# Performance work log

Measured on AMD Instinct MI355X. Metric: run time of the kernel, lower is better.

Reference implementation:

```python
import jax, jax.numpy as jnp
import numpy as np

EPS = 1e-5
NHEAD = 8

def layernorm(x, g, b):
    m = x.mean(-1, keepdims=True)
    v = ((x - m) ** 2).mean(-1, keepdims=True)
    return (x - m) * jax.lax.rsqrt(v + EPS) * g + b


def setup_inputs() -> dict:
    key = jax.random.key(0)
    ks = jax.random.split(key, 20)
    D, F, K, G, NC, FF, B = 768, 2048, 100, 10, 1000, 2048, 128
    s = lambda k, shape, scale: jax.random.normal(k, shape, jnp.float32) * scale
    return {
        "x": s(ks[0], (B, F, 7, 7), 1.0),
        "W_embed": s(ks[1], (F, D), 0.02), "b_embed": jnp.zeros((D,), jnp.float32),
        "query_embed": s(ks[2], (K, D), 1.0),
        "wq": s(ks[3], (D, D), 0.03), "wk": s(ks[4], (D, D), 0.03), "wv": s(ks[5], (D, D), 0.03),
        "bq": jnp.zeros((D,), jnp.float32), "bk": jnp.zeros((D,), jnp.float32), "bv": jnp.zeros((D,), jnp.float32),
        "wo": s(ks[6], (D, D), 0.03), "bo": jnp.zeros((D,), jnp.float32),
        "w1": s(ks[7], (D, FF), 0.03), "b1": jnp.zeros((FF,), jnp.float32),
        "w2": s(ks[8], (FF, D), 0.02), "b2": jnp.zeros((D,), jnp.float32),
        "g1": jnp.ones((D,), jnp.float32), "be1": jnp.zeros((D,), jnp.float32),
        "g2": jnp.ones((D,), jnp.float32), "be2": jnp.zeros((D,), jnp.float32),
        "g3": jnp.ones((D,), jnp.float32), "be3": jnp.zeros((D,), jnp.float32),
        "dup_pool": s(ks[9], (K, D, G), 0.03),
        "dup_bias": jnp.zeros((NC,), jnp.float32),
    }


def reference(x, W_embed, b_embed, query_embed, wq, wk, wv, bq, bk, bv, wo, bo,
              w1, b1, w2, b2, g1, be1, g2, be2, g3, be3, dup_pool, dup_bias):
    B = x.shape[0]
    D = W_embed.shape[1]
    H = NHEAD
    hd = D // H
    num_classes = dup_bias.shape[0]

    # [B, 2048, 7, 7] -> [B, 49, 2048] -> [B, 49, 768], relu
    mem = x.reshape(B, x.shape[1], -1).transpose(0, 2, 1)
    mem = jax.nn.relu(mem @ W_embed + b_embed)          # (B, S, D)

    # queries broadcast to batch (batch-first internally)
    tgt = jnp.broadcast_to(query_embed[None], (B,) + query_embed.shape)  # (B, K, D)

    # tgt = tgt + dropout1(tgt) -> 2*tgt in eval; then norm1
    tgt = layernorm(2.0 * tgt, g1, be1)

    # cross multi-head attention: Q=tgt, K=V=mem
    q = (tgt @ wq + bq).reshape(B, -1, H, hd)
    k = (mem @ wk + bk).reshape(B, -1, H, hd)
    v = (mem @ wv + bv).reshape(B, -1, H, hd)
    scores = jnp.einsum("bkhd,bshd->bhks", q, k) / jnp.sqrt(jnp.float32(hd))
    attn = jax.nn.softmax(scores, axis=-1)
    ctx = jnp.einsum("bhks,bshd->bkhd", attn, v).reshape(B, -1, D)
    attn_out = ctx @ wo + bo

    tgt = layernorm(tgt + attn_out, g2, be2)

    # FFN
    ff = jax.nn.relu(tgt @ w1 + b1) @ w2 + b2
    h = layernorm(tgt + ff, g3, be3)                    # (B, K, D)

    # GroupFC: per-group matmul, batched as one einsum
    out_extrap = jnp.einsum("bkd,kdg->bkg", h, dup_pool)  # (B, K, G)
    logits = out_extrap.reshape(B, -1)[:, :num_classes] + dup_bias
    return logits
```

## Files before the change

### kernel.cpp

```cpp
#include <hip/hip_runtime.h>
#include <math.h>

#define D_MODEL 768
#define HEADS   8
#define HDIM    96
#define SEQ     49
#define KQ      100
#define NB      128
#define FDIM    2048
#define FFD     2048
#define GRP     10
#define NCLS    1000

typedef unsigned short ushort_t;
typedef unsigned int uint_t;
typedef __attribute__((ext_vector_type(8))) short short8;
typedef __attribute__((ext_vector_type(4))) float f32x4;

__device__ __forceinline__ float bf2f(ushort_t u) {
    uint_t x = ((uint_t)u) << 16;
    return __uint_as_float(x);
}
__device__ __forceinline__ ushort_t f2bf(float f) {
    uint_t x = __float_as_uint(f);
    x += 0x7fffu + ((x >> 16) & 1u);
    return (ushort_t)(x >> 16);
}

__device__ __forceinline__ void gld_lds16(const void* g, void* l) {
    __builtin_amdgcn_global_load_lds(
        (const __attribute__((address_space(1))) unsigned int*)g,
        (__attribute__((address_space(3))) unsigned int*)l, 16, 0, 0);
}

template <int MT>
__device__ __forceinline__ void gemm_body(
    const ushort_t* __restrict__ A, const ushort_t* __restrict__ Bt,
    const float* __restrict__ bias, const float* __restrict__ bias2,
    ushort_t* __restrict__ C, ushort_t* __restrict__ C2,
    int M, int N, int K, int nsplit, int relu, float scale,
    const ushort_t* __restrict__ resid, int rmode, int r, int c)
{
    constexpr int BM  = MT * 32;
    constexpr int ACH = MT * 4;
    constexpr int NCH = (ACH + 16) / 4;
    constexpr int CTS = 132;

    __shared__ ushort_t smem[BM * 64 + 128 * 64];
    ushort_t* As = smem;
    ushort_t* Bs = smem + BM * 64;

    const int tid  = threadIdx.x;
    const int w    = tid >> 6;
    const int lane = tid & 63;
    const int quad = lane >> 4;
    const int l16  = lane & 15;

    const int rowBase = r * BM;
    const int nBase   = c * 128;
    const int wr = (w >> 1) * (MT * 16);
    const int wc = (w & 1) * 64;

    const float* biasb;
    ushort_t* Cb;
    int coff, ldcb;
    if (nBase < nsplit) { biasb = bias;  Cb = C;  coff = 0;      ldcb = nsplit; }
    else                { biasb = bias2; Cb = C2; coff = nsplit; ldcb = N - nsplit; }

    f32x4 acc[MT][4];
#pragma unroll
    for (int i = 0; i < MT; i++)
#pragma unroll
        for (int j = 0; j < 4; j++) acc[i][j] = (f32x4){0.f, 0.f, 0.f, 0.f};

    const int lrow = lane >> 3;
    const int ksub = ((lane & 7) ^ ((lane >> 3) & 7)) * 8;

    const ushort_t* gp[NCH];
    ushort_t* lp[NCH];
#pragma unroll
    for (int i = 0; i < NCH; i++) {
        int ch = w + 4 * i;
        if (ch < ACH) {
            int rr = min(rowBase + ch * 8 + lrow, M - 1);
            gp[i] = A + (size_t)rr * K + ksub;
            lp[i] = As + ch * 512 + lane * 8;
        } else {
            int cb = ch - ACH;
            int rr = nBase + cb * 8 + lrow;
            gp[i] = Bt + (size_t)rr * K + ksub;
            lp[i] = Bs + cb * 512 + lane * 8;
        }
    }

    const int swl = l16 & 7;

    for (int k0 = 0; k0 < K; k0 += 64) {
#pragma unroll
        for (int i = 0; i < NCH; i++) gld_lds16(gp[i] + k0, lp[i]);
        __syncthreads();

#pragma unroll
        for (int s = 0; s < 2; s++) {
            const int ks = ((4 * s + quad) ^ swl) * 8;
            short8 af[MT], bfr[4];
#pragma unroll
            for (int mt = 0; mt < MT; mt++)
                af[mt] = *(const short8*)(As + (wr + mt * 16 + l16) * 64 + ks);
#pragma unroll
            for (int nt = 0; nt < 4; nt++)
                bfr[nt] = *(const short8*)(Bs + (wc + nt * 16 + l16) * 64 + ks);
#pragma unroll
            for (int mt = 0; mt < MT; mt++)
#pragma unroll
                for (int nt = 0; nt < 4; nt++)
                    acc[mt][nt] = __builtin_amdgcn_mfma_f32_16x16x32_bf16(
                        af[mt], bfr[nt], acc[mt][nt], 0, 0, 0);
        }
        __syncthreads();
    }

    ushort_t* Ct = smem;
#pragma unroll
    for (int nt = 0; nt < 4; nt++) {
        const int colg = nBase + wc + nt * 16 + l16;
        const int col  = colg - coff;
        const float bv = biasb[col];
#pragma unroll
        for (int mt = 0; mt < MT; mt++) {
#pragma unroll
            for (int rg = 0; rg < 4; rg++) {
                const int lr  = wr + mt * 16 + quad * 4 + rg;
                const int row = rowBase + lr;
                float v = (acc[mt][nt][rg] + bv) * scale;
                if (relu) v = fmaxf(v, 0.f);
                if (rmode && row < M) {
                    int rrow = (rmode == 2) ? (row % KQ) : row;
                    v += bf2f(resid[(size_t)rrow * D_MODEL + col]);
                }
                Ct[lr * CTS + wc + nt * 16 + l16] = f2bf(v);
            }
        }
    }
    __syncthreads();

    const int ocol = (tid & 15) * 8;
    const int ceff = nBase - coff + ocol;
#pragma unroll
    for (int i = 0; i < BM / 16; i++) {
        const int lr  = i * 16 + (tid >> 4);
        const int row = rowBase + lr;
        if (row < M) {
            short8 vv = *(const short8*)(Ct + lr * CTS + ocol);
            *(short8*)(Cb + (size_t)row * ldcb + ceff) = vv;
        }
    }
}

__device__ __forceinline__ void xcd_remap(int bx, int by, int nx, int NY,
                                          int& r, int& c)
{
    const int bid = by * nx + bx;
    const int NYmain = NY & ~7;
    const int Tmain = NYmain * nx;
    if (bid < Tmain) {
        const int grp = bid / (8 * nx);
        const int rem = bid - grp * 8 * nx;
        r = grp * 8 + (rem & 7);
        c = rem >> 3;
    } else {
        const int rem = bid - Tmain;
        r = NYmain + rem / nx;
        c = rem - (rem / nx) * nx;
    }
}

template <int MT>
__global__ __launch_bounds__(256, 4) void gemm_bf16(
    const ushort_t* __restrict__ A, const ushort_t* __restrict__ Bt,
    const float* __restrict__ bias, const float* __restrict__ bias2,
    ushort_t* __restrict__ C, ushort_t* __restrict__ C2,
    int M, int N, int K, int nsplit, int relu, float scale,
    const ushort_t* __restrict__ resid, int rmode)
{
    int r, c;
    xcd_remap(blockIdx.x, blockIdx.y, gridDim.x, gridDim.y, r, c);
    gemm_body<MT>(A, Bt, bias, bias2, C, C2, M, N, K, nsplit, relu, scale,
                  resid, rmode, r, c);
}

__global__ __launch_bounds__(256, 4) void gemm_kv_qb(
    const ushort_t* __restrict__ mem, const ushort_t* __restrict__ wkt,
    const float* __restrict__ bk, const float* __restrict__ bv,
    ushort_t* __restrict__ kb, ushort_t* __restrict__ vb,
    const ushort_t* __restrict__ tgt, const ushort_t* __restrict__ wqt,
    const float* __restrict__ bq, ushort_t* __restrict__ qb,
    float qscale)
{
    const int bx = blockIdx.x, by = blockIdx.y;
    const ushort_t *A, *Bt;
    const float *bias, *bias2;
    ushort_t *C, *C2;
    int M, N, K, ns, r, c;
    float scale;
    if (by < 98) {
        xcd_remap(bx, by, 12, 98, r, c);
        A = mem; Bt = wkt; bias = bk; bias2 = bv; C = kb; C2 = vb;
        M = 6272; N = 1536; K = 768; ns = 768; scale = 1.f;
    } else {
        if (bx >= 6) return;
        r = by - 98; c = bx;
        A = tgt; Bt = wqt; bias = bq; bias2 = bq; C = qb; C2 = qb;
        M = KQ; N = 768; K = 768; ns = 768; scale = qscale;
    }
    gemm_body<2>(A, Bt, bias, bias2, C, C2, M, N, K, ns, 0, scale,
                 nullptr, 0, r, c);
}

__global__ __launch_bounds__(256) void prep_all(
    const float* __restrict__ We, const float* __restrict__ wq,
    const float* __restrict__ wk, const float* __restrict__ wv,
    const float* __restrict__ wo, const float* __restrict__ w1,
    const float* __restrict__ w2, const float* __restrict__ x,
    ushort_t* __restrict__ Wet, ushort_t* __restrict__ wqt,
    ushort_t* __restrict__ wkt, ushort_t* __restrict__ wvt,
    ushort_t* __restrict__ wot, ushort_t* __restrict__ w1t,
    ushort_t* __restrict__ w2t, ushort_t* __restrict__ xb,
    const float* __restrict__ qe, const float* __restrict__ g1,
    const float* __restrict__ be1, ushort_t* __restrict__ tgt)
{
    __shared__ __align__(16) char smem[25600];
    int t = blockIdx.x;
    if (t < 1728) {
        float* tile = (float*)smem;
        const float* src; ushort_t* dst; int K, N, tx;
        if (t < 384)       {           src = We; dst = Wet; K = 2048; N = 768;  tx = 12; }
        else if (t < 528)  { t -= 384; src = wq; dst = wqt; K = 768;  N = 768;  tx = 12; }
        else if (t < 672)  { t -= 528; src = wk; dst = wkt; K = 768;  N = 768;  tx = 12; }
        else if (t < 816)  { t -= 672; src = wv; dst = wvt; K = 768;  N = 768;  tx = 12; }
        else if (t < 960)  { t -= 816; src = wo; dst = wot; K = 768;  N = 768;  tx = 12; }
        else if (t < 1344) { t -= 960; src = w1; dst = w1t; K = 768;  N = 2048; tx = 32; }
        else               { t -= 1344; src = w2; dst = w2t; K = 2048; N = 768; tx = 12; }
        const int n0 = (t % tx) * 64, k0 = (t / tx) * 64;
        const int tr = threadIdx.x >> 6, tc = threadIdx.x & 63;
#pragma unroll
        for (int i = 0; i < 16; i++) {
            int r = i * 4 + tr;
            tile[r * 65 + tc] = src[(size_t)(k0 + r) * N + n0 + tc];
        }
        __syncthreads();
#pragma unroll
        for (int it = 0; it < 2; it++) {
            const int u  = threadIdx.x + it * 256;
            const int nr = u >> 3, ch = (u & 7) * 8;
            short8 v;
#pragma unroll
            for (int j = 0; j < 8; j++)
                v[j] = (short)f2bf(tile[(ch + j) * 65 + nr]);
            *(short8*)(dst + (size_t)(n0 + nr) * K + k0 + ch) = v;
        }
    } else if (t < 2752) {
        ushort_t* tile = (ushort_t*)smem;
        int bx = t - 1728;
        const int b = bx >> 3, f0 = (bx & 7) * 256, tt = threadIdx.x;
        const float* src = x + ((size_t)b * FDIM + f0 + tt) * SEQ;
#pragma unroll
        for (int s = 0; s < SEQ; s++) tile[tt * 50 + s] = f2bf(src[s]);
        __syncthreads();
#pragma unroll
        for (int it = 0; it < 7; it++) {
            const int u = tt + it * 256;
            if (u < SEQ * 32) {
                const int s = u >> 5, ch = (u & 31) * 8;
                short8 v;
#pragma unroll
                for (int j = 0; j < 8; j++)
                    v[j] = (short)tile[(ch + j) * 50 + s];
                *(short8*)(xb + (size_t)(b * SEQ + s) * FDIM + f0 + ch) = v;
            }
        }
    } else {
        const int w = threadIdx.x >> 6, lane = threadIdx.x & 63;
        const int row = (t - 2752) * 4 + w;
        if (row >= KQ) return;

        float v[12];
        const float2* p = (const float2*)(qe + (size_t)row * D_MODEL);
#pragma unroll
        for (int i = 0; i < 6; i++) {
            float2 tv = p[lane + i * 64];
            v[2 * i]     = tv.x * 2.0f;
            v[2 * i + 1] = tv.y * 2.0f;
        }
        float s = 0.f;
#pragma unroll
        for (int i = 0; i < 12; i++) s += v[i];
#pragma unroll
        for (int off = 32; off > 0; off >>= 1) s += __shfl_xor(s, off);
        const float mean = s * (1.f / D_MODEL);
        float q = 0.f;
#pragma unroll
        for (int i = 0; i < 12; i++) { float d = v[i] - mean; q += d * d; }
#pragma unroll
        for (int off = 32; off > 0; off >>= 1) q += __shfl_xor(q, off);
        const float rstd = rsqrtf(q * (1.f / D_MODEL) + 1e-5f);

        const float2* g2 = (const float2*)g1;
        const float2* b2 = (const float2*)be1;
        uint_t* op = (uint_t*)tgt + (size_t)row * 384;
#pragma unroll
        for (int i = 0; i < 6; i++) {
            int j = lane + i * 64;
            float2 gg = g2[j], bb = b2[j];
            ushort_t lo = f2bf((v[2 * i] - mean) * rstd * gg.x + bb.x);
            ushort_t hi = f2bf((v[2 * i + 1] - mean) * rstd * gg.y + bb.y);
            op[j] = (uint_t)lo | ((uint_t)hi << 16);
        }
    }
}

__global__ __launch_bounds__(256) void ln4(
    const void* __restrict__ in, int in_bf16,
    const float* __restrict__ g, const float* __restrict__ be,
    ushort_t* __restrict__ out, float pre_scale, int nrows)
{
    const int w = threadIdx.x >> 6, lane = threadIdx.x & 63;
    const int row = blockIdx.x * 4 + w;
    if (row >= nrows) return;

    float v[12];
    if (in_bf16) {
        const uint_t* p = (const uint_t*)in + (size_t)row * 384;
#pragma unroll
        for (int i = 0; i < 6; i++) {
            uint_t u = p[lane + i * 64];
            v[2 * i]     = bf2f((ushort_t)(u & 0xffff)) * pre_scale;
            v[2 * i + 1] = bf2f((ushort_t)(u >> 16)) * pre_scale;
        }
    } else {
        const float2* p = (const float2*)((const float*)in + (size_t)row * D_MODEL);
#pragma unroll
        for (int i = 0; i < 6; i++) {
            float2 t = p[lane + i * 64];
            v[2 * i] = t.x * pre_scale;
            v[2 * i + 1] = t.y * pre_scale;
        }
    }
    float s = 0.f;
#pragma unroll
    for (int i = 0; i < 12; i++) s += v[i];
#pragma unroll
    for (int off = 32; off > 0; off >>= 1) s += __shfl_xor(s, off);
    const float mean = s * (1.f / D_MODEL);
    float q = 0.f;
#pragma unroll
    for (int i = 0; i < 12; i++) { float d = v[i] - mean; q += d * d; }
#pragma unroll
    for (int off = 32; off > 0; off >>= 1) q += __shfl_xor(q, off);
    const float rstd = rsqrtf(q * (1.f / D_MODEL) + 1e-5f);

    const float2* g2 = (const float2*)g;
    const float2* b2 = (const float2*)be;
    uint_t* op = (uint_t*)out + (size_t)row * 384;
#pragma unroll
    for (int i = 0; i < 6; i++) {
        int j = lane + i * 64;
        float2 gg = g2[j], bb = b2[j];
        ushort_t lo = f2bf((v[2 * i] - mean) * rstd * gg.x + bb.x);
        ushort_t hi = f2bf((v[2 * i + 1] - mean) * rstd * gg.y + bb.y);
        op[j] = (uint_t)lo | ((uint_t)hi << 16);
    }
}

__global__ __launch_bounds__(256) void attn_mfma(
    const ushort_t* __restrict__ q, const ushort_t* __restrict__ k,
    const ushort_t* __restrict__ v, ushort_t* __restrict__ ctx)
{
    __shared__ ushort_t Pt[128][72];
    __shared__ ushort_t Vt[96][72];

    const int bh = blockIdx.x;
    const int b = bh >> 3, h = bh & 7;
    const int tid = threadIdx.x;
    const int w = tid >> 6, lane = tid & 63;
    const int quad = lane >> 4, l16 = lane & 15;
    const int mrow0 = 32 * w;

    for (int idx = tid; idx < 96 * 64; idx += 256) {
        int d = idx >> 6, s = idx & 63;
        ushort_t val = 0;
        if (s < SEQ) val = v[(size_t)(b * SEQ + s) * D_MODEL + h * HDIM + d];
        Vt[d][s] = val;
    }

    f32x4 accS[2][4];
#pragma unroll
    for (int i = 0; i < 2; i++)
#pragma unroll
        for (int j = 0; j < 4; j++) accS[i][j] = (f32x4){0.f, 0.f, 0.f, 0.f};

#pragma unroll
    for (int k0 = 0; k0 < HDIM; k0 += 32) {
        short8 af[2], bfr[4];
#pragma unroll
        for (int mt = 0; mt < 2; mt++) {
            int kq = min(mrow0 + mt * 16 + l16, KQ - 1);
            af[mt] = *(const short8*)(q + (size_t)kq * D_MODEL + h * HDIM + k0 + quad * 8);
        }
#pragma unroll
        for (int nt = 0; nt < 4; nt++) {
            int s = min(nt * 16 + l16, SEQ - 1);
            bfr[nt] = *(const short8*)(k + (size_t)(b * SEQ + s) * D_MODEL + h * HDIM + k0 + quad * 8);
        }
#pragma unroll
        for (int mt = 0; mt < 2; mt++)
#pragma unroll
            for (int nt = 0; nt < 4; nt++)
                accS[mt][nt] = __builtin_amdgcn_mfma_f32_16x16x32_bf16(
                    af[mt], bfr[nt], accS[mt][nt], 0, 0, 0);
    }

#pragma unroll
    for (int mt = 0; mt < 2; mt++) {
#pragma unroll
        for (int r = 0; r < 4; r++) {
            float vals[4];
            float vmax = -1e30f;
#pragma unroll
            for (int nt = 0; nt < 4; nt++) {
                vals[nt] = accS[mt][nt][r];
                if (nt * 16 + l16 < SEQ) vmax = fmaxf(vmax, vals[nt]);
            }
#pragma unroll
            for (int off = 1; off < 16; off <<= 1)
                vmax = fmaxf(vmax, __shfl_xor(vmax, off));
            float p[4], psum = 0.f;
#pragma unroll
            for (int nt = 0; nt < 4; nt++) {
                float e = (nt * 16 + l16 < SEQ) ? __expf(vals[nt] - vmax) : 0.f;
                p[nt] = e;
                psum += e;
            }
#pragma unroll
            for (int off = 1; off < 16; off <<= 1)
                psum += __shfl_xor(psum, off);
            const float inv = 1.f / psum;
            const int row = mrow0 + mt * 16 + quad * 4 + r;
#pragma unroll
            for (int nt = 0; nt < 4; nt++)
                Pt[row][nt * 16 + l16] = f2bf(p[nt] * inv);
        }
    }
    __syncthreads();

    f32x4 accO[2][6];
#pragma unroll
    for (int i = 0; i < 2; i++)
#pragma unroll
        for (int j = 0; j < 6; j++) accO[i][j] = (f32x4){0.f, 0.f, 0.f, 0.f};

#pragma unroll
    for (int k0 = 0; k0 < 64; k0 += 32) {
        short8 af[2], bfr[6];
#pragma unroll
        for (int mt = 0; mt < 2; mt++)
            af[mt] = *(const short8*)(&Pt[mrow0 + mt * 16 + l16][k0 + quad * 8]);
#pragma unroll
        for (int nt = 0; nt < 6; nt++)
            bfr[nt] = *(const short8*)(&Vt[nt * 16 + l16][k0 + quad * 8]);
#pragma unroll
        for (int mt = 0; mt < 2; mt++)
#pragma unroll
            for (int nt = 0; nt < 6; nt++)
                accO[mt][nt] = __builtin_amdgcn_mfma_f32_16x16x32_bf16(
                    af[mt], bfr[nt], accO[mt][nt], 0, 0, 0);
    }

#pragma unroll
    for (int mt = 0; mt < 2; mt++) {
#pragma unroll
        for (int r = 0; r < 4; r++) {
            const int kq = mrow0 + mt * 16 + quad * 4 + r;
            if (kq < KQ) {
                size_t oa = (size_t)(b * KQ + kq) * D_MODEL + h * HDIM;
#pragma unroll
                for (int nt = 0; nt < 6; nt++)
                    ctx[oa + nt * 16 + l16] = f2bf(accO[mt][nt][r]);
            }
        }
    }
}

__global__ __launch_bounds__(256) void groupfc3(
    const ushort_t* __restrict__ hb, const float* __restrict__ dp,
    const float* __restrict__ dbias, const float* __restrict__ g3,
    const float* __restrict__ be3, float* __restrict__ out)
{
    __shared__ float dps[D_MODEL * 11];
    __shared__ float hsr[8][D_MODEL];
    __shared__ float gbs[2][D_MODEL];

    const int b0 = blockIdx.x * 8;
    const int kq = blockIdx.y;
    const int tid = threadIdx.x;

    for (int i = tid; i < D_MODEL * GRP; i += 256) {
        int d = i / GRP, g = i - d * GRP;
        dps[d * 11 + g] = dp[(size_t)kq * (D_MODEL * GRP) + i];
    }
    for (int i = tid; i < D_MODEL; i += 256) {
        gbs[0][i] = g3[i];
        gbs[1][i] = be3[i];
    }
#pragma unroll
    for (int bb = 0; bb < 8; bb++) {
#pragma unroll
        for (int i = 0; i < 3; i++) {
            int d = tid + i * 256;
            hsr[bb][d] = bf2f(hb[(size_t)((b0 + bb) * KQ + kq) * D_MODEL + d]);
        }
    }
    __syncthreads();

    const int w = tid >> 6, lane = tid & 63;

#pragma unroll
    for (int rr = 0; rr < 2; rr++) {
        const int r = w * 2 + rr;
        float v[12];
        float s = 0.f;
#pragma unroll
        for (int i = 0; i < 12; i++) { v[i] = hsr[r][lane + i * 64]; s += v[i]; }
#pragma unroll
        for (int off = 32; off > 0; off >>= 1) s += __shfl_xor(s, off);
        const float mean = s * (1.f / D_MODEL);
        float q = 0.f;
#pragma unroll
        for (int i = 0; i < 12; i++) { float d = v[i] - mean; q += d * d; }
#pragma unroll
        for (int off = 32; off > 0; off >>= 1) q += __shfl_xor(q, off);
        const float rstd = rsqrtf(q * (1.f / D_MODEL) + 1e-5f);
#pragma unroll
        for (int i = 0; i < 12; i++) {
            int d = lane + i * 64;
            hsr[r][d] = (v[i] - mean) * rstd * gbs[0][d] + gbs[1][d];
        }
    }
    __syncthreads();

    for (int item = w; item < 8 * GRP; item += 4) {
        int bb = item / GRP, g = item - bb * GRP;
        float a = 0.f;
#pragma unroll
        for (int i = 0; i < 12; i++) {
            int d = lane + i * 64;
            a = fmaf(hsr[bb][d], dps[d * 11 + g], a);
        }
#pragma unroll
        for (int off = 32; off > 0; off >>= 1) a += __shfl_down(a, off);
        if (lane == 0)
            out[(size_t)(b0 + bb) * NCLS + kq * GRP + g] = a + dbias[kq * GRP + g];
    }
}

extern "C" void kernel_launch(void* const* d_in, const int* in_sizes, int n_in,
                              void* d_out, int out_size, void* d_ws, size_t ws_size,
                              hipStream_t stream)
{
    const float* x   = (const float*)d_in[0];
    const float* We  = (const float*)d_in[1];
    const float* be_ = (const float*)d_in[2];
    const float* qe  = (const float*)d_in[3];
    const float* wq  = (const float*)d_in[4];
    const float* wk  = (const float*)d_in[5];
    const float* wv  = (const float*)d_in[6];
    const float* bq  = (const float*)d_in[7];
    const float* bk  = (const float*)d_in[8];
    const float* bv  = (const float*)d_in[9];
    const float* wo  = (const float*)d_in[10];
    const float* bo  = (const float*)d_in[11];
    const float* w1  = (const float*)d_in[12];
    const float* b1  = (const float*)d_in[13];
    const float* w2  = (const float*)d_in[14];
    const float* b2  = (const float*)d_in[15];
    const float* g1  = (const float*)d_in[16];
    const float* be1 = (const float*)d_in[17];
    const float* g2  = (const float*)d_in[18];
    const float* be2 = (const float*)d_in[19];
    const float* g3  = (const float*)d_in[20];
    const float* be3 = (const float*)d_in[21];
    const float* dp  = (const float*)d_in[22];
    const float* db  = (const float*)d_in[23];
    float* out = (float*)d_out;
    ushort_t* ws = (ushort_t*)d_ws;

    ushort_t* xb  = ws;
    ushort_t* mem = xb + 12845056;
    ushort_t* kb  = mem + 4816896;
    ushort_t* vb  = kb + 4816896;
    ushort_t* ffh = ws;
    ushort_t* rB  = ws + 27295744;
    ushort_t* Wet = rB;
    ushort_t* wqt = Wet + 1572864;
    ushort_t* wkt = wqt + 589824;
    ushort_t* wvt = wkt + 589824;
    ushort_t* wot = wvt + 589824;
    ushort_t* w1t = wot + 589824;
    ushort_t* w2t = w1t + 1572864;
    ushort_t* tgt = w2t + 1572864;
    ushort_t* qb  = tgt + 76800;
    ushort_t* ctx = qb + 76800;
    ushort_t* t2  = ctx + 9830400;
    ushort_t* hb  = t2 + 9830400;

    dim3 blk(256);
    const float qscale = 1.0f / sqrtf((float)HDIM);

    prep_all<<<dim3(2777), blk, 0, stream>>>(We, wq, wk, wv, wo, w1, w2, x,
                                             Wet, wqt, wkt, wvt, wot, w1t, w2t, xb,
                                             qe, g1, be1, tgt);

    gemm_bf16<2><<<dim3(6, 98), blk, 0, stream>>>(xb, Wet, be_, be_, mem, mem,
                                                  6272, 768, 2048, 768, 1, 1.f, nullptr, 0);
    gemm_kv_qb<<<dim3(12, 100), blk, 0, stream>>>(mem, wkt, bk, bv, kb, vb,
                                                  tgt, wqt, bq, qb, qscale);
    attn_mfma<<<dim3(NB * HEADS), blk, 0, stream>>>(qb, kb, vb, ctx);
    gemm_bf16<2><<<dim3(6, 200), blk, 0, stream>>>(ctx, wot, bo, bo, t2, t2,
                                                   12800, 768, 768, 768, 0, 1.f, tgt, 2);
    ln4<<<dim3(3200), blk, 0, stream>>>(t2, 1, g2, be2, t2, 1.0f, 12800);
    gemm_bf16<2><<<dim3(16, 200), blk, 0, stream>>>(t2, w1t, b1, b1, ffh, ffh,
                                                    12800, 2048, 768, 2048, 1, 1.f, nullptr, 0);
    gemm_bf16<2><<<dim3(6, 200), blk, 0, stream>>>(ffh, w2t, b2, b2, hb, hb,
                                                   12800, 768, 2048, 768, 0, 1.f, t2, 1);
    groupfc3<<<dim3(16, KQ), blk, 0, stream>>>(hb, dp, db, g3, be3, out);
}
```

Before: 446.7 us.

## Double-buffer GEMM LDS tiles to overlap global loads with MFMA

Doubles the shared-memory allocation so the next K-tile is loaded directly into LDS while the MFMA loop consumes the current one. Explicit vmcnt waits and raw barriers replace the __syncthreads pairs, so compute is meant to overlap with global-to-LDS transfer latency. In exchange, LDS usage doubles, which may reduce occupancy, and correctness now depends on hand-written waitcnt counts.

```diff
diff --git a/kernel.cpp b/kernel.cpp
--- a/kernel.cpp
+++ b/kernel.cpp
@@ -45,10 +45,9 @@
     constexpr int ACH = MT * 4;
     constexpr int NCH = (ACH + 16) / 4;
     constexpr int CTS = 132;
-
-    __shared__ ushort_t smem[BM * 64 + 128 * 64];
-    ushort_t* As = smem;
-    ushort_t* Bs = smem + BM * 64;
+    constexpr int BUF = BM * 64 + 128 * 64;
+
+    __shared__ ushort_t smem[2 * BUF];
 
     const int tid  = threadIdx.x;
     const int w    = tid >> 6;
@@ -77,29 +76,44 @@
     const int ksub = ((lane & 7) ^ ((lane >> 3) & 7)) * 8;
 
     const ushort_t* gp[NCH];
-    ushort_t* lp[NCH];
+    int lpo[NCH];
 #pragma unroll
     for (int i = 0; i < NCH; i++) {
         int ch = w + 4 * i;
         if (ch < ACH) {
             int rr = min(rowBase + ch * 8 + lrow, M - 1);
-            gp[i] = A + (size_t)rr * K + ksub;
-            lp[i] = As + ch * 512 + lane * 8;
+            gp[i]  = A + (size_t)rr * K + ksub;
+            lpo[i] = ch * 512 + lane * 8;
         } else {
             int cb = ch - ACH;
             int rr = nBase + cb * 8 + lrow;
-            gp[i] = Bt + (size_t)rr * K + ksub;
-            lp[i] = Bs + cb * 512 + lane * 8;
+            gp[i]  = Bt + (size_t)rr * K + ksub;
+            lpo[i] = BM * 64 + cb * 512 + lane * 8;
         }
     }
 
     const int swl = l16 & 7;
-
-    for (int k0 = 0; k0 < K; k0 += 64) {
-#pragma unroll
-        for (int i = 0; i < NCH; i++) gld_lds16(gp[i] + k0, lp[i]);
-        __syncthreads();
-
+    const int NT  = K >> 6;
+
+#pragma unroll
+    for (int i = 0; i < NCH; i++) gld_lds16(gp[i], smem + lpo[i]);
+
+    for (int t = 0; t < NT; ++t) {
+        const ushort_t* cur = smem + (t & 1) * BUF;
+        ushort_t* nxt = smem + ((t + 1) & 1) * BUF;
+
+        if (t + 1 < NT) {
+#pragma unroll
+            for (int i = 0; i < NCH; i++)
+                gld_lds16(gp[i] + (size_t)(t + 1) * 64, nxt + lpo[i]);
+            asm volatile("s_waitcnt vmcnt(%0)" :: "n"(NCH) : "memory");
+        } else {
+            asm volatile("s_waitcnt vmcnt(0)" ::: "memory");
+        }
+        __builtin_amdgcn_s_barrier();
+
+        const ushort_t* As = cur;
+        const ushort_t* Bs = cur + BM * 64;
 #pragma unroll
         for (int s = 0; s < 2; s++) {
             const int ks = ((4 * s + quad) ^ swl) * 8;
@@ -117,7 +131,8 @@
                     acc[mt][nt] = __builtin_amdgcn_mfma_f32_16x16x32_bf16(
                         af[mt], bfr[nt], acc[mt][nt], 0, 0, 0);
         }
-        __syncthreads();
+        asm volatile("s_waitcnt lgkmcnt(0)" ::: "memory");
+        __builtin_amdgcn_s_barrier();
     }
 
     ushort_t* Ct = smem;
```

Measured after the change: 464.3 us. 1.04x slower.
